# Performance work log

Measured on AMD Instinct MI355X. Metric: run time of the kernel, lower is better.

The kernel has to match this reference:

```python
import jax, jax.numpy as jnp
import numpy as np
import math

KH = KW = 3
STRIDE = 1
PAD = 1
DIL = 1
C_IN = 256
C_OUT = 256
RANK = 32
BATCH = 16
H = W = 56


def setup_inputs() -> dict:
    key = jax.random.key(0)
    kx, kg, kh_, kb = jax.random.split(key, 4)
    x = jax.random.normal(kx, (BATCH, C_IN, H, W), dtype=jnp.float32)
    k2 = KH * KW
    bg = 1.0 / math.sqrt(C_IN)
    bh = 1.0 / math.sqrt(RANK)
    G = jax.random.uniform(kg, (k2, RANK, C_IN), minval=-bg, maxval=bg, dtype=jnp.float32)
    Hm = jax.random.uniform(kh_, (k2, C_OUT, RANK), minval=-bh, maxval=bh, dtype=jnp.float32)
    bias = jax.random.uniform(kb, (C_OUT,), minval=-bg, maxval=bg, dtype=jnp.float32)
    return {"x": x, "G": G, "Hm": Hm, "bias": bias}


def reference(x, G, Hm, bias):
    # Low-rank conv: per kernel position k, project patch through G[k] (rank) then H[k] (out),
    # then MEAN over the k2 positions (matches the original's .mean(dim=0)).
    b, c, h, w = x.shape
    h_out = (h + 2 * PAD - DIL * (KH - 1) - 1) // STRIDE + 1
    w_out = (h + 2 * PAD - DIL * (KW - 1) - 1) // STRIDE + 1  # original uses h here; square input
    xp = jnp.pad(x, ((0, 0), (0, 0), (PAD, PAD), (PAD, PAD)))
    acc = jnp.zeros((b, Hm.shape[1], h_out, w_out), dtype=x.dtype)
    for i in range(KH):
        for j in range(KW):
            k = i * KW + j
            # strided patch view for kernel offset (i, j): [b, c, h_out, w_out]
            patch = xp[:, :,
                       i * DIL:i * DIL + (h_out - 1) * STRIDE + 1:STRIDE,
                       j * DIL:j * DIL + (w_out - 1) * STRIDE + 1:STRIDE]
            t = jnp.einsum('bchw,rc->brhw', patch, G[k])      # rank projection
            acc = acc + jnp.einsum('brhw,or->bohw', t, Hm[k])  # out projection
    out = acc / (KH * KW) + bias[None, :, None, None]
    return out
```

## Files before the change

### kernel.cpp

```cpp
#include <hip/hip_runtime.h>
#include <stdint.h>


#define BATCH 16
#define CIN   256
#define COUT  256
#define RANK  32
#define HH    56
#define WW    56
#define SP    (HH*WW)
#define NPOS  (BATCH*SP)
#define YP    58
#define XP    58
#define PCELL (YP*XP)
#define PLANE (BATCH*PCELL)

typedef __bf16 bf16x8 __attribute__((ext_vector_type(8)));
typedef float  f32x4  __attribute__((ext_vector_type(4)));

#define OFF_XT 0
#define OFF_T9 25690112
#define OFF_GB (OFF_T9 + 31002624)
#define OFF_HB (OFF_GB + 147456)

__device__ __forceinline__ uint16_t bfbits(float f) {
  __bf16 h = (__bf16)f;
  return __builtin_bit_cast(uint16_t, h);
}

__global__ __launch_bounds__(256) void k_wcast(const float* __restrict__ G,
                                               const float* __restrict__ Hm,
                                               uint16_t* __restrict__ G_bf,
                                               uint16_t* __restrict__ Hm_bf) {
  int i = blockIdx.x * 256 + threadIdx.x;
  if (i < 73728) G_bf[i] = bfbits(G[i]);
  else           Hm_bf[i - 73728] = bfbits(Hm[i - 73728]);
}

#define RING_U4 (9 * 16 * 228 * 4)
__global__ __launch_bounds__(256) void k_ring(uint16_t* __restrict__ T9) {
  int i = blockIdx.x * 256 + threadIdx.x;
  if (i >= RING_U4) return;
  int v = i & 3, cell = i >> 2;
  int tb = cell / 228, c = cell % 228;
  int y, x;
  if      (c < 58)  { y = 0;       x = c;       }
  else if (c < 116) { y = 57;      x = c - 58;  }
  else if (c < 172) { y = c - 115; x = 0;       }
  else              { y = c - 171; x = 57;      }
  uint16_t* base = T9 + ((size_t)tb * PCELL + y * XP + x) * 32;
  uint4 z; z.x = z.y = z.z = z.w = 0u;
  ((uint4*)base)[v] = z;
}

__global__ __launch_bounds__(256) void k_transpose(const float* __restrict__ x,
                                                   uint16_t* __restrict__ x_t) {
  __shared__ float tile[64][65];
  const int b = blockIdx.z, c0 = blockIdx.y * 64, s0 = blockIdx.x * 64;
  const int a = threadIdx.x & 63, g = threadIdx.x >> 6;
#pragma unroll
  for (int r = 0; r < 16; ++r) {
    int c = g * 16 + r;
    tile[c][a] = x[((size_t)(b * CIN + c0 + c)) * SP + s0 + a];
  }
  __syncthreads();
#pragma unroll
  for (int r = 0; r < 16; ++r) {
    int s = g * 16 + r;
    x_t[((size_t)(b * SP + s0 + s)) * CIN + c0 + a] = bfbits(tile[a][s]);
  }
}

__global__ __launch_bounds__(384, 3) void k_stage1(const uint16_t* __restrict__ G_bf,
                                                   const uint16_t* __restrict__ x_t,
                                                   uint16_t* __restrict__ T9) {
  const int wave = threadIdx.x >> 6, lane = threadIdx.x & 63;
  const int q = lane >> 4, t = lane & 15;

  bf16x8 A[3][8];
  {
    const uint16_t* gb = G_bf + ((size_t)(wave * 48 + t)) * CIN + q * 8;
#pragma unroll
    for (int i = 0; i < 3; ++i)
#pragma unroll
      for (int ks = 0; ks < 8; ++ks)
        A[i][ks] = *(const bf16x8*)(gb + (size_t)i * 16 * CIN + ks * 32);
  }

#pragma unroll 1
  for (int item = blockIdx.x; item < 1568; item += 512) {
    const int b = item & 15, ch = item >> 4;
#pragma unroll 1
    for (int it = 0; it < 2; ++it) {
      const int p = ch * 32 + it * 16 + t;
      const uint16_t* xb = x_t + ((size_t)b * SP + p) * CIN + q * 8;
      bf16x8 Bf[8];
#pragma unroll
      for (int ks = 0; ks < 8; ++ks)
        Bf[ks] = *(const bf16x8*)(xb + ks * 32);

      f32x4 acc[3];
#pragma unroll
      for (int i = 0; i < 3; ++i) acc[i] = (f32x4){0.f, 0.f, 0.f, 0.f};
#pragma unroll
      for (int ks = 0; ks < 8; ++ks)
#pragma unroll
        for (int i = 0; i < 3; ++i)
          acc[i] = __builtin_amdgcn_mfma_f32_16x16x32_bf16(A[i][ks], Bf[ks], acc[i], 0, 0, 0);

      const int h = p / WW, w = p - (p / WW) * WW;
      const size_t cellbase = ((size_t)b * PCELL + (h + 1) * XP + (w + 1)) * 32;
#pragma unroll
      for (int i = 0; i < 3; ++i) {
        const int kr0 = wave * 48 + i * 16 + q * 4;
        const int tap = kr0 >> 5, r = kr0 & 31;
        uint2 pv;
        pv.x = (uint32_t)bfbits(acc[i][0]) | ((uint32_t)bfbits(acc[i][1]) << 16);
        pv.y = (uint32_t)bfbits(acc[i][2]) | ((uint32_t)bfbits(acc[i][3]) << 16);
        *(uint2*)(T9 + (size_t)tap * PLANE * 32 + cellbase + r) = pv;
      }
    }
  }
}

__global__ __launch_bounds__(256, 2) void k_stage2(const uint16_t* __restrict__ T9,
                                                   const uint16_t* __restrict__ Hm_bf,
                                                   const float* __restrict__ bias,
                                                   float* __restrict__ out) {
  const int wave = threadIdx.x >> 6, lane = threadIdx.x & 63;
  const int q = lane >> 4, t = lane & 15;

  bf16x8 Bf[9][4];
  float bv[4];
#pragma unroll
  for (int j = 0; j < 4; ++j) {
    const int o = wave * 64 + j * 16 + t;
    bv[j] = bias[o];
#pragma unroll
    for (int tap = 0; tap < 9; ++tap)
      Bf[tap][j] = *(const bf16x8*)(Hm_bf + ((size_t)(tap * COUT + o)) * RANK + q * 8);
  }

#pragma unroll 1
  for (int mt = blockIdx.x; mt < 3136; mt += 512) {
    const int p0 = mt * 16;
    const int b = p0 / SP, s0 = p0 - b * SP;
    const int sa = s0 + t;
    const int ha = sa / WW, wa = sa - ha * WW;
    const uint16_t* abase = T9 + ((size_t)(b * PCELL + ha * XP + wa)) * 32 + q * 8;

    f32x4 acc[4];
#pragma unroll
    for (int j = 0; j < 4; ++j) acc[j] = (f32x4){0.f, 0.f, 0.f, 0.f};

#pragma unroll
    for (int tap = 0; tap < 9; ++tap) {
      const int di = tap / 3, dj = tap % 3;
      bf16x8 af = *(const bf16x8*)(abase + (size_t)tap * PLANE * 32 + (di * XP + dj) * 32);
#pragma unroll
      for (int j = 0; j < 4; ++j)
        acc[j] = __builtin_amdgcn_mfma_f32_16x16x32_bf16(af, Bf[tap][j], acc[j], 0, 0, 0);
    }

    const int sd = s0 + q * 4;
#pragma unroll
    for (int j = 0; j < 4; ++j) {
      const int o = wave * 64 + j * 16 + t;
      f32x4 v = acc[j] * (1.0f / 9.0f) + bv[j];
      *(f32x4*)(out + ((size_t)(b * COUT + o)) * SP + sd) = v;
    }
  }
}

extern "C" void kernel_launch(void* const* d_in, const int* in_sizes, int n_in,
                              void* d_out, int out_size, void* d_ws, size_t ws_size,
                              hipStream_t stream) {
  const float* x    = (const float*)d_in[0];
  const float* G    = (const float*)d_in[1];
  const float* Hm   = (const float*)d_in[2];
  const float* bias = (const float*)d_in[3];
  float* out = (float*)d_out;
  char* ws = (char*)d_ws;

  uint16_t* x_t   = (uint16_t*)(ws + OFF_XT);
  uint16_t* T9    = (uint16_t*)(ws + OFF_T9);
  uint16_t* G_bf  = (uint16_t*)(ws + OFF_GB);
  uint16_t* Hm_bf = (uint16_t*)(ws + OFF_HB);

  k_wcast<<<576, 256, 0, stream>>>(G, Hm, G_bf, Hm_bf);
  k_ring<<<(RING_U4 + 255) / 256, 256, 0, stream>>>(T9);
  k_transpose<<<dim3(49, 4, 16), 256, 0, stream>>>(x, x_t);
  k_stage1<<<512, 384, 0, stream>>>(G_bf, x_t, T9);
  k_stage2<<<512, 256, 0, stream>>>(T9, Hm_bf, bias, out);
}
```

Baseline: 156.6 us.

## Fuse input transpose into stage1 via LDS staging, merge prep kernels, widen stage2

Removes the separate transpose kernel that wrote a bf16 channel-last copy of x. Stage1 now reads fp32 x directly, converts each 32-position by 256-channel tile to bf16 in shared memory, then runs the rank-projection MFMAs from LDS. The weight cast and ring-zeroing kernels are merged into a single prep launch. Stage2 moves to 512-thread blocks with each wave covering 32 output channels instead of 64, which lowers register pressure and raises occupancy but reloads each T9 fragment across more waves.

```diff
diff --git a/kernel.cpp b/kernel.cpp
--- a/kernel.cpp
+++ b/kernel.cpp
@@ -9,7 +9,6 @@
 #define HH    56
 #define WW    56
 #define SP    (HH*WW)
-#define NPOS  (BATCH*SP)
 #define YP    58
 #define XP    58
 #define PCELL (YP*XP)
@@ -18,68 +17,51 @@
 typedef __bf16 bf16x8 __attribute__((ext_vector_type(8)));
 typedef float  f32x4  __attribute__((ext_vector_type(4)));
 
-#define OFF_XT 0
-#define OFF_T9 25690112
-#define OFF_GB (OFF_T9 + 31002624)
+#define OFF_T9 0
+#define OFF_GB 31002624
 #define OFF_HB (OFF_GB + 147456)
+
+#define RING_U4 (9 * 16 * 228 * 4)
+#define PREP_N  (147456 + RING_U4)
 
 __device__ __forceinline__ uint16_t bfbits(float f) {
   __bf16 h = (__bf16)f;
   return __builtin_bit_cast(uint16_t, h);
 }
 
-__global__ __launch_bounds__(256) void k_wcast(const float* __restrict__ G,
-                                               const float* __restrict__ Hm,
-                                               uint16_t* __restrict__ G_bf,
-                                               uint16_t* __restrict__ Hm_bf) {
+__global__ __launch_bounds__(256) void k_prep(const float* __restrict__ G,
+                                              const float* __restrict__ Hm,
+                                              uint16_t* __restrict__ G_bf,
+                                              uint16_t* __restrict__ Hm_bf,
+                                              uint16_t* __restrict__ T9) {
   int i = blockIdx.x * 256 + threadIdx.x;
-  if (i < 73728) G_bf[i] = bfbits(G[i]);
-  else           Hm_bf[i - 73728] = bfbits(Hm[i - 73728]);
-}
-
-#define RING_U4 (9 * 16 * 228 * 4)
-__global__ __launch_bounds__(256) void k_ring(uint16_t* __restrict__ T9) {
-  int i = blockIdx.x * 256 + threadIdx.x;
-  if (i >= RING_U4) return;
-  int v = i & 3, cell = i >> 2;
+  if (i < 73728)  { G_bf[i] = bfbits(G[i]); return; }
+  if (i < 147456) { Hm_bf[i - 73728] = bfbits(Hm[i - 73728]); return; }
+  int j = i - 147456;
+  if (j >= RING_U4) return;
+  int v = j & 3, cell = j >> 2;
   int tb = cell / 228, c = cell % 228;
-  int y, x;
-  if      (c < 58)  { y = 0;       x = c;       }
-  else if (c < 116) { y = 57;      x = c - 58;  }
-  else if (c < 172) { y = c - 115; x = 0;       }
-  else              { y = c - 171; x = 57;      }
-  uint16_t* base = T9 + ((size_t)tb * PCELL + y * XP + x) * 32;
+  int y, xx;
+  if      (c < 58)  { y = 0;       xx = c;       }
+  else if (c < 116) { y = 57;      xx = c - 58;  }
+  else if (c < 172) { y = c - 115; xx = 0;       }
+  else              { y = c - 171; xx = 57;      }
+  uint16_t* base = T9 + ((size_t)tb * PCELL + y * XP + xx) * 32;
   uint4 z; z.x = z.y = z.z = z.w = 0u;
   ((uint4*)base)[v] = z;
 }
 
-__global__ __launch_bounds__(256) void k_transpose(const float* __restrict__ x,
-                                                   uint16_t* __restrict__ x_t) {
-  __shared__ float tile[64][65];
-  const int b = blockIdx.z, c0 = blockIdx.y * 64, s0 = blockIdx.x * 64;
-  const int a = threadIdx.x & 63, g = threadIdx.x >> 6;
-#pragma unroll
-  for (int r = 0; r < 16; ++r) {
-    int c = g * 16 + r;
-    tile[c][a] = x[((size_t)(b * CIN + c0 + c)) * SP + s0 + a];
-  }
-  __syncthreads();
-#pragma unroll
-  for (int r = 0; r < 16; ++r) {
-    int s = g * 16 + r;
-    x_t[((size_t)(b * SP + s0 + s)) * CIN + c0 + a] = bfbits(tile[a][s]);
-  }
-}
-
-__global__ __launch_bounds__(384, 3) void k_stage1(const uint16_t* __restrict__ G_bf,
-                                                   const uint16_t* __restrict__ x_t,
+__global__ __launch_bounds__(384, 3) void k_fused1(const float* __restrict__ x,
+                                                   const uint16_t* __restrict__ G_bf,
                                                    uint16_t* __restrict__ T9) {
-  const int wave = threadIdx.x >> 6, lane = threadIdx.x & 63;
+  __shared__ uint16_t xs[32 * 264];
+  const int tid = threadIdx.x;
+  const int wave = tid >> 6, lane = tid & 63;
   const int q = lane >> 4, t = lane & 15;
 
   bf16x8 A[3][8];
   {
-    const uint16_t* gb = G_bf + ((size_t)(wave * 48 + t)) * CIN + q * 8;
+    const uint16_t* gb = G_bf + (size_t)(wave * 48 + t) * CIN + q * 8;
 #pragma unroll
     for (int i = 0; i < 3; ++i)
 #pragma unroll
@@ -89,15 +71,26 @@
 
 #pragma unroll 1
   for (int item = blockIdx.x; item < 1568; item += 512) {
-    const int b = item & 15, ch = item >> 4;
+    const int b = item / 98, ch = item - b * 98;
+
 #pragma unroll 1
-    for (int it = 0; it < 2; ++it) {
-      const int p = ch * 32 + it * 16 + t;
-      const uint16_t* xb = x_t + ((size_t)b * SP + p) * CIN + q * 8;
+    for (int u = tid; u < 1024; u += 384) {
+      const int s = u & 31, cg = u >> 5;
+      const float* xr = x + ((size_t)(b * CIN + cg * 8)) * SP + ch * 32 + s;
+      bf16x8 v;
+#pragma unroll
+      for (int e = 0; e < 8; ++e)
+        ((__bf16*)&v)[e] = (__bf16)xr[(size_t)e * SP];
+      *(bf16x8*)&xs[s * 264 + cg * 8] = v;
+    }
+    __syncthreads();
+
+#pragma unroll 1
+    for (int nt = 0; nt < 2; ++nt) {
       bf16x8 Bf[8];
 #pragma unroll
       for (int ks = 0; ks < 8; ++ks)
-        Bf[ks] = *(const bf16x8*)(xb + ks * 32);
+        Bf[ks] = *(const bf16x8*)&xs[(nt * 16 + t) * 264 + ks * 32 + q * 8];
 
       f32x4 acc[3];
 #pragma unroll
@@ -108,6 +101,7 @@
         for (int i = 0; i < 3; ++i)
           acc[i] = __builtin_amdgcn_mfma_f32_16x16x32_bf16(A[i][ks], Bf[ks], acc[i], 0, 0, 0);
 
+      const int p = ch * 32 + nt * 16 + t;
       const int h = p / WW, w = p - (p / WW) * WW;
       const size_t cellbase = ((size_t)b * PCELL + (h + 1) * XP + (w + 1)) * 32;
 #pragma unroll
@@ -120,21 +114,22 @@
         *(uint2*)(T9 + (size_t)tap * PLANE * 32 + cellbase + r) = pv;
       }
     }
+    __syncthreads();
   }
 }
 
-__global__ __launch_bounds__(256, 2) void k_stage2(const uint16_t* __restrict__ T9,
+__global__ __launch_bounds__(512, 4) void k_stage2(const uint16_t* __restrict__ T9,
                                                    const uint16_t* __restrict__ Hm_bf,
                                                    const float* __restrict__ bias,
                                                    float* __restrict__ out) {
   const int wave = threadIdx.x >> 6, lane = threadIdx.x & 63;
   const int q = lane >> 4, t = lane & 15;
 
-  bf16x8 Bf[9][4];
-  float bv[4];
+  bf16x8 Bf[9][2];
+  float bv[2];
 #pragma unroll
-  for (int j = 0; j < 4; ++j) {
-    const int o = wave * 64 + j * 16 + t;
+  for (int j = 0; j < 2; ++j) {
+    const int o = wave * 32 + j * 16 + t;
     bv[j] = bias[o];
 #pragma unroll
     for (int tap = 0; tap < 9; ++tap)
@@ -149,23 +144,21 @@
     const int ha = sa / WW, wa = sa - ha * WW;
     const uint16_t* abase = T9 + ((size_t)(b * PCELL + ha * XP + wa)) * 32 + q * 8;
 
-    f32x4 acc[4];
-#pragma unroll
-    for (int j = 0; j < 4; ++j) acc[j] = (f32x4){0.f, 0.f, 0.f, 0.f};
-
+    f32x4 acc[2];
+    acc[0] = (f32x4){0.f, 0.f, 0.f, 0.f};
+    acc[1] = (f32x4){0.f, 0.f, 0.f, 0.f};
 #pragma unroll
     for (int tap = 0; tap < 9; ++tap) {
       const int di = tap / 3, dj = tap % 3;
       bf16x8 af = *(const bf16x8*)(abase + (size_t)tap * PLANE * 32 + (di * XP + dj) * 32);
-#pragma unroll
-      for (int j = 0; j < 4; ++j)
-        acc[j] = __builtin_amdgcn_mfma_f32_16x16x32_bf16(af, Bf[tap][j], acc[j], 0, 0, 0);
+      acc[0] = __builtin_amdgcn_mfma_f32_16x16x32_bf16(af, Bf[0 + tap][0], acc[0], 0, 0, 0);
+      acc[1] = __builtin_amdgcn_mfma_f32_16x16x32_bf16(af, Bf[0 + tap][1], acc[1], 0, 0, 0);
     }
 
     const int sd = s0 + q * 4;
 #pragma unroll
-    for (int j = 0; j < 4; ++j) {
-      const int o = wave * 64 + j * 16 + t;
+    for (int j = 0; j < 2; ++j) {
+      const int o = wave * 32 + j * 16 + t;
       f32x4 v = acc[j] * (1.0f / 9.0f) + bv[j];
       *(f32x4*)(out + ((size_t)(b * COUT + o)) * SP + sd) = v;
     }
@@ -182,14 +175,11 @@
   float* out = (float*)d_out;
   char* ws = (char*)d_ws;
 
-  uint16_t* x_t   = (uint16_t*)(ws + OFF_XT);
   uint16_t* T9    = (uint16_t*)(ws + OFF_T9);
   uint16_t* G_bf  = (uint16_t*)(ws + OFF_GB);
   uint16_t* Hm_bf = (uint16_t*)(ws + OFF_HB);
 
-  k_wcast<<<576, 256, 0, stream>>>(G, Hm, G_bf, Hm_bf);
-  k_ring<<<(RING_U4 + 255) / 256, 256, 0, stream>>>(T9);
-  k_transpose<<<dim3(49, 4, 16), 256, 0, stream>>>(x, x_t);
-  k_stage1<<<512, 384, 0, stream>>>(G_bf, x_t, T9);
-  k_stage2<<<512, 256, 0, stream>>>(T9, Hm_bf, bias, out);
+  k_prep<<<PREP_N / 256, 256, 0, stream>>>(G, Hm, G_bf, Hm_bf, T9);
+  k_fused1<<<512, 384, 0, stream>>>(x, G_bf, T9);
+  k_stage2<<<512, 512, 0, stream>>>(T9, Hm_bf, bias, out);
 }
```

Measured after the change: 142.6 us. 1.1x faster.
